# Optimization experiments

Hardware: AMD Instinct MI355X
Metric: run time of the kernel (lower is better)

## Reference

```python
import jax, jax.numpy as jnp
import numpy as np

N = 100000      # num nodes
E = 1600000     # num edges (no self-loops; forward appends N self-loops)
DIN = 256       # in_channels
H = 1           # heads
C = 64          # out_channels per head
NEG = 0.2       # leaky_relu negative slope
NID = N // 10   # number of ID nodes


def setup_inputs() -> dict:
    key = jax.random.key(0)
    ks = jax.random.split(key, 7)
    x = jax.random.normal(ks[0], (N, DIN), jnp.float32)
    src = jax.random.randint(ks[1], (E,), 0, N, dtype=jnp.int32)
    off = jax.random.randint(ks[2], (E,), 1, N, dtype=jnp.int32)
    dst = ((src.astype(jnp.int64) + off.astype(jnp.int64)) % N).astype(jnp.int32)  # guarantees no self-loops
    edge_index = jnp.stack([src, dst])  # [2, E], row0 = source j, row1 = target i
    node_id = jax.random.randint(ks[3], (NID,), 0, N, dtype=jnp.int32)
    g = float(1.0 / np.sqrt(DIN))  # glorot-ish scale
    W = jax.random.uniform(ks[4], (DIN, H * C), jnp.float32, -g, g)
    W_id = jax.random.uniform(ks[5], (DIN, H * C), jnp.float32, -g, g)
    att = jax.random.uniform(ks[6], (1, H, 2 * C), jnp.float32, -g, g)
    return dict(x=x, edge_index=edge_index, node_id=node_id, W=W, W_id=W_id, att=att)


def _gat_id_forward(x, W, W_id, att, edge_index, node_id):
    # ID-aware transform: x @ W, plus extra W_id contribution added at id nodes
    x_id = x[node_id] @ W_id                      # [NID, H*C]
    h = x @ W                                     # [N, H*C]
    h = h.at[node_id].add(x_id)
    # add self-loops (inputs contain none)
    loops = jnp.arange(N, dtype=edge_index.dtype)
    src = jnp.concatenate([edge_index[0], loops])  # source j
    dst = jnp.concatenate([edge_index[1], loops])  # target i
    hr = h.reshape(N, H, C)
    xi = hr[dst]                                   # [Et, H, C]
    xj = hr[src]                                   # [Et, H, C]
    # alpha = (cat(x_i, x_j) * att).sum(-1)
    alpha = (xi * att[:, :, :C]).sum(-1) + (xj * att[:, :, C:]).sum(-1)  # [Et, H]
    alpha = jax.nn.leaky_relu(alpha, NEG)
    # segment softmax over target node (every node has a self-loop -> no empty segments)
    m = jax.ops.segment_max(alpha, dst, num_segments=N)
    alpha = jnp.exp(alpha - m[dst])
    s = jax.ops.segment_sum(alpha, dst, num_segments=N)
    alpha = alpha / (s[dst] + 1e-16)
    # dropout p=0 / eval mode -> no-op
    out = jax.ops.segment_sum(xj * alpha[:, :, None], dst, num_segments=N)  # [N, H, C]
    return out.reshape(N, H * C)  # concat=True, bias=False


def reference(x, edge_index, node_id, W, W_id, att):
    return _gat_id_forward(x, W, W_id, att, edge_index, node_id)
```

## Files before the change

### kernel.cpp

```cpp
#include <hip/hip_runtime.h>
#include <hip/hip_bf16.h>

#define N_NODES 100000
#define E_EDGES 1600000
#define DIN 256
#define C_OUT 64
#define NID_CNT 10000
#define NEG 0.2f
#define NBUCK 391
#define CAP 4608
#define GEMM_BLOCKS 782
#define BIN_BLOCKS 242
#define BIN_EPB 6612
#define ID_BLOCKS 79

typedef short bf16x8 __attribute__((ext_vector_type(8)));
typedef float f32x4  __attribute__((ext_vector_type(4)));

__device__ __forceinline__ float lrelu(float x) { return x > 0.f ? x : NEG * x; }
__device__ __forceinline__ unsigned short f2bs(float f) {
    __hip_bfloat16 b = __float2bfloat16(f);
    return *reinterpret_cast<unsigned short*>(&b);
}
__device__ __forceinline__ bf16x8 pack8(float4 a, float4 b) {
    bf16x8 r;
    r[0] = (short)f2bs(a.x); r[1] = (short)f2bs(a.y);
    r[2] = (short)f2bs(a.z); r[3] = (short)f2bs(a.w);
    r[4] = (short)f2bs(b.x); r[5] = (short)f2bs(b.y);
    r[6] = (short)f2bs(b.z); r[7] = (short)f2bs(b.w);
    return r;
}
__device__ __forceinline__ float2 unpk2(unsigned u) {
    return make_float2(__uint_as_float(u << 16), __uint_as_float(u & 0xffff0000u));
}

__global__ __launch_bounds__(256) void k_zero(float* __restrict__ cnt,
                                              int* __restrict__ bkcur) {
    const int t = blockIdx.x * 256 + threadIdx.x;
    if (t < N_NODES) cnt[t] = 0.f;
    if (t < NBUCK) bkcur[t] = t * CAP;
}

__global__ __launch_bounds__(256) void k_prep(const float* __restrict__ W,
                                              const float* __restrict__ Wid,
                                              unsigned short* __restrict__ WtG,
                                              unsigned short* __restrict__ WidtG,
                                              const int* __restrict__ nid,
                                              float* __restrict__ cnt) {
    const int b = blockIdx.x;
    const int tid = threadIdx.x;
    if (b < 128) {
        const int t = b * 256 + tid;
        const int mat = t >> 14;
        const int r = t & 16383;
        const int k = r >> 6, c = r & 63;
        if (mat == 0) WtG[c * DIN + k] = f2bs(W[(long)k * C_OUT + c]);
        else          WidtG[c * DIN + k] = f2bs(Wid[(long)k * C_OUT + c]);
    } else {
        const int t = (b - 128) * 256 + tid;
        if (t < NID_CNT) atomicAdd(&cnt[nid[t]], 1.0f);
    }
}

__global__ __launch_bounds__(512, 8) void k_mega(const float* __restrict__ x,
                                                 const unsigned short* __restrict__ WtG,
                                                 const float* __restrict__ att,
                                                 __hip_bfloat16* __restrict__ hb,
                                                 float* __restrict__ ad,
                                                 float* __restrict__ as,
                                                 const int* __restrict__ ei,
                                                 int* __restrict__ bkcur,
                                                 int2* __restrict__ binned) {
    __shared__ __align__(16) char smem[32768];
    const int blk = blockIdx.x;
    const int tid = threadIdx.x;

    if (blk < GEMM_BLOCKS) {
        char* wlds = smem;
        const int w = tid >> 6, l = tid & 63;
        const int g = l >> 4, cl = l & 15;
        const int r0 = blk * 128;

        #pragma unroll
        for (int i = 0; i < 4; ++i) {
            int f = tid + i * 512;
            int c = f >> 5, s = f & 31;
            int byte = c * 512 + ((s ^ (c & 7)) << 4);
            *(bf16x8*)(wlds + byte) = *(const bf16x8*)(WtG + (long)c * DIN + s * 8);
        }
        __syncthreads();

        f32x4 acc[4] = {};
        const int row0 = r0 + w * 16 + cl;
        const float* xp0 = x + (long)min(row0, N_NODES - 1) * DIN + g * 8;

        float4 xb[2][2];
        xb[0][0] = *(const float4*)(xp0);
        xb[0][1] = *(const float4*)(xp0 + 4);
        #pragma unroll
        for (int kt = 0; kt < 8; ++kt) {
            if (kt < 7) {
                const int nb = (kt + 1) & 1;
                xb[nb][0] = *(const float4*)(xp0 + (kt + 1) * 32);
                xb[nb][1] = *(const float4*)(xp0 + (kt + 1) * 32 + 4);
            }
            const int cb = kt & 1;
            bf16x8 a0 = pack8(xb[cb][0], xb[cb][1]);
            #pragma unroll
            for (int ct = 0; ct < 4; ++ct) {
                int c = ct * 16 + cl;
                int byte = c * 512 + (((kt * 4 + g) ^ (c & 7)) << 4);
                bf16x8 bw = *(const bf16x8*)(wlds + byte);
                acc[ct] = __builtin_amdgcn_mfma_f32_16x16x32_bf16(a0, bw, acc[ct], 0, 0, 0);
            }
        }
        __syncthreads();

        float attv1[4], attv2[4];
        #pragma unroll
        for (int ct = 0; ct < 4; ++ct) {
            attv1[ct] = att[ct * 16 + cl];
            attv2[ct] = att[C_OUT + ct * 16 + cl];
        }
        unsigned short* hbt = (unsigned short*)smem;
        #pragma unroll
        for (int reg = 0; reg < 4; ++reg) {
            const int rbl = w * 16 + g * 4 + reg;
            float pd = 0.f, ps = 0.f;
            #pragma unroll
            for (int ct = 0; ct < 4; ++ct) {
                float hv = acc[ct][reg];
                pd += hv * attv1[ct];
                ps += hv * attv2[ct];
                hbt[rbl * 72 + ct * 16 + cl] = f2bs(hv);
            }
            #pragma unroll
            for (int o = 1; o < 16; o <<= 1) {
                pd += __shfl_xor(pd, o, 64);
                ps += __shfl_xor(ps, o, 64);
            }
            if (cl == 0) {
                int grow = r0 + rbl;
                if (grow < N_NODES) { ad[grow] = pd; as[grow] = ps; }
            }
        }
        __syncthreads();
        #pragma unroll
        for (int i = 0; i < 2; ++i) {
            int f = tid + i * 512;
            int row = f >> 3, s = f & 7;
            int grow = r0 + row;
            if (grow < N_NODES) {
                bf16x8 v = *(const bf16x8*)(smem + row * 144 + s * 16);
                *(bf16x8*)((unsigned short*)hb + (long)grow * C_OUT + s * 8) = v;
            }
        }
    } else {
        int* cnt_s = (int*)smem;
        int* base  = cnt_s + NBUCK;
        int* lcur  = base + NBUCK;
        const int b2 = blk - GEMM_BLOCKS;
        const int e0 = b2 * BIN_EPB;
        const int e1 = min(e0 + BIN_EPB, E_EDGES);
        for (int i = tid; i < NBUCK; i += 512) cnt_s[i] = 0;
        __syncthreads();
        for (int e = e0 + tid; e < e1; e += 512)
            atomicAdd(&cnt_s[ei[E_EDGES + e] >> 8], 1);
        __syncthreads();
        for (int i = tid; i < NBUCK; i += 512) {
            base[i] = cnt_s[i] ? atomicAdd(&bkcur[i], cnt_s[i]) : 0;
            lcur[i] = 0;
        }
        __syncthreads();
        for (int e = e0 + tid; e < e1; e += 512) {
            int s = ei[e];
            int d = ei[E_EDGES + e];
            int bb = d >> 8;
            int r = atomicAdd(&lcur[bb], 1);
            binned[base[bb] + r] = make_int2(s, d);
        }
    }
}

__global__ __launch_bounds__(256) void k_gemm_id(const float* __restrict__ x,
                                                 const unsigned short* __restrict__ WtG,
                                                 const unsigned short* __restrict__ WidtG,
                                                 const float* __restrict__ cnt,
                                                 const int* __restrict__ nid,
                                                 const float* __restrict__ att,
                                                 __hip_bfloat16* __restrict__ hb,
                                                 float* __restrict__ ad,
                                                 float* __restrict__ as) {
    __shared__ __align__(16) char wlds[65536];
    __shared__ int nodes[128];
    __shared__ float cvs[128];
    const int tid = threadIdx.x;
    const int w = tid >> 6, l = tid & 63;
    const int g = l >> 4, cl = l & 15;
    const int r0 = blockIdx.x * 128;
    if (tid < 128) {
        int idx = r0 + tid;
        int nd = (idx < NID_CNT) ? nid[idx] : -1;
        nodes[tid] = nd;
        cvs[tid] = (nd >= 0) ? cnt[nd] : 0.f;
    }
    #pragma unroll
    for (int i = 0; i < 16; ++i) {
        int f = tid + i * 256;
        int half = f >> 11;
        int ff = f & 2047;
        int c = ff >> 5, s = ff & 31;
        int byte = half * 32768 + c * 512 + ((s ^ (c & 7)) << 4);
        const unsigned short* src = half ? WidtG : WtG;
        *(bf16x8*)(wlds + byte) = *(const bf16x8*)(src + (long)c * DIN + s * 8);
    }
    __syncthreads();

    const int n0 = nodes[w * 32 + cl];
    const int n1 = nodes[w * 32 + 16 + cl];
    const float* xp0 = x + (long)max(n0, 0) * DIN + g * 8;
    const float* xp1 = x + (long)max(n1, 0) * DIN + g * 8;

    f32x4 acc1[2][4] = {};
    f32x4 acc2[2][4] = {};
    #pragma unroll
    for (int kt = 0; kt < 8; ++kt) {
        float4 u0 = *(const float4*)(xp0 + kt * 32);
        float4 u1 = *(const float4*)(xp0 + kt * 32 + 4);
        float4 v0 = *(const float4*)(xp1 + kt * 32);
        float4 v1 = *(const float4*)(xp1 + kt * 32 + 4);
        bf16x8 a0 = pack8(u0, u1);
        bf16x8 a1 = pack8(v0, v1);
        #pragma unroll
        for (int ct = 0; ct < 4; ++ct) {
            int c = ct * 16 + cl;
            int byte = c * 512 + (((kt * 4 + g) ^ (c & 7)) << 4);
            bf16x8 bw = *(const bf16x8*)(wlds + byte);
            bf16x8 bi = *(const bf16x8*)(wlds + 32768 + byte);
            acc1[0][ct] = __builtin_amdgcn_mfma_f32_16x16x32_bf16(a0, bw, acc1[0][ct], 0, 0, 0);
            acc1[1][ct] = __builtin_amdgcn_mfma_f32_16x16x32_bf16(a1, bw, acc1[1][ct], 0, 0, 0);
            acc2[0][ct] = __builtin_amdgcn_mfma_f32_16x16x32_bf16(a0, bi, acc2[0][ct], 0, 0, 0);
            acc2[1][ct] = __builtin_amdgcn_mfma_f32_16x16x32_bf16(a1, bi, acc2[1][ct], 0, 0, 0);
        }
    }
    __syncthreads();

    float attv1[4], attv2[4];
    #pragma unroll
    for (int ct = 0; ct < 4; ++ct) {
        attv1[ct] = att[ct * 16 + cl];
        attv2[ct] = att[C_OUT + ct * 16 + cl];
    }
    unsigned short* hbt = (unsigned short*)wlds;
    #pragma unroll
    for (int rt = 0; rt < 2; ++rt) {
        #pragma unroll
        for (int reg = 0; reg < 4; ++reg) {
            const int rbl = w * 32 + rt * 16 + g * 4 + reg;
            const float cv = cvs[rbl];
            float pd = 0.f, ps = 0.f;
            #pragma unroll
            for (int ct = 0; ct < 4; ++ct) {
                float hv = acc1[rt][ct][reg] + cv * acc2[rt][ct][reg];
                pd += hv * attv1[ct];
                ps += hv * attv2[ct];
                hbt[rbl * 72 + ct * 16 + cl] = f2bs(hv);
            }
            #pragma unroll
            for (int o = 1; o < 16; o <<= 1) {
                pd += __shfl_xor(pd, o, 64);
                ps += __shfl_xor(ps, o, 64);
            }
            if (cl == 0) {
                int nd = nodes[rbl];
                if (nd >= 0) { ad[nd] = pd; as[nd] = ps; }
            }
        }
    }
    __syncthreads();
    #pragma unroll
    for (int i = 0; i < 4; ++i) {
        int f = tid + i * 256;
        int row = f >> 3, s = f & 7;
        int nd = nodes[row];
        if (nd >= 0) {
            bf16x8 v = *(const bf16x8*)(wlds + row * 144 + s * 16);
            *(bf16x8*)((unsigned short*)hb + (long)nd * C_OUT + s * 8) = v;
        }
    }
}

__global__ __launch_bounds__(256) void k_place(const int2* __restrict__ binned,
                                               const int* __restrict__ bkcur,
                                               int* __restrict__ csr,
                                               int* __restrict__ cur) {
    __shared__ int ncnt[256];
    __shared__ int tmp[256];
    __shared__ int ncur[256];
    const int tid = threadIdx.x;
    const int b = blockIdx.x;
    const int lo = b * CAP;
    const int n = bkcur[b] - lo;
    const int node0 = b << 8;
    ncnt[tid] = 0;
    __syncthreads();
    for (int e = tid; e < n; e += 256)
        atomicAdd(&ncnt[binned[lo + e].y - node0], 1);
    __syncthreads();
    const int v = ncnt[tid];
    tmp[tid] = v;
    __syncthreads();
    for (int o = 1; o < 256; o <<= 1) {
        int t = (tid >= o) ? tmp[tid - o] : 0;
        __syncthreads();
        tmp[tid] += t;
        __syncthreads();
    }
    const int incl = tmp[tid];
    if (node0 + tid < N_NODES) cur[node0 + tid] = lo + incl;
    ncur[tid] = incl - v;
    __syncthreads();
    for (int e = tid; e < n; e += 256) {
        int2 p = binned[lo + e];
        int r = atomicAdd(&ncur[p.y - node0], 1);
        csr[lo + r] = p.x;
    }
}

__global__ __launch_bounds__(256) void k_gather(const int* __restrict__ cur,
                                                const int* __restrict__ csr,
                                                const unsigned* __restrict__ hb2,
                                                const float* __restrict__ ad,
                                                const float* __restrict__ as,
                                                float* __restrict__ out) {
    const int lane = threadIdx.x & 63;
    const int lg = lane & 31;
    const int gb = lane & 32;
    const int i = blockIdx.x * 8 + ((threadIdx.x >> 6) << 1) + (lane >> 5);
    if (i >= N_NODES) return;
    const int end   = cur[i];
    const int start = (i & 255) ? cur[i - 1] : (i >> 8) * CAP;
    const int deg   = end - start;
    const float adi = ad[i];
    const float asi = as[i];
    float2 acc;
    float den;
    if (deg <= 32) {
        int s = 0; float a = -1e30f;
        if (lg < deg) { s = csr[start + lg]; a = as[s]; }
        float mx = fmaxf(a, asi);
        #pragma unroll
        for (int o = 16; o > 0; o >>= 1) mx = fmaxf(mx, __shfl_xor(mx, o, 64));
        const float m = lrelu(adi + mx);
        float w = (lg < deg) ? __expf(lrelu(adi + a) - m) : 0.f;
        const float wself = __expf(lrelu(adi + asi) - m);
        float wsum = w;
        #pragma unroll
        for (int o = 16; o > 0; o >>= 1) wsum += __shfl_xor(wsum, o, 64);
        den = wself + wsum;
        float2 hv = unpk2(hb2[(long)i * 32 + lg]);
        acc = make_float2(wself * hv.x, wself * hv.y);
        int j = 0;
        for (; j + 4 <= deg; j += 4) {
            int   s0 = __shfl(s, gb + j, 64),     s1 = __shfl(s, gb + j + 1, 64),
                  s2 = __shfl(s, gb + j + 2, 64), s3 = __shfl(s, gb + j + 3, 64);
            float w0 = __shfl(w, gb + j, 64),     w1 = __shfl(w, gb + j + 1, 64),
                  w2 = __shfl(w, gb + j + 2, 64), w3 = __shfl(w, gb + j + 3, 64);
            float2 h0 = unpk2(hb2[(long)s0 * 32 + lg]);
            float2 h1 = unpk2(hb2[(long)s1 * 32 + lg]);
            float2 h2 = unpk2(hb2[(long)s2 * 32 + lg]);
            float2 h3 = unpk2(hb2[(long)s3 * 32 + lg]);
            acc.x += w0 * h0.x; acc.y += w0 * h0.y;
            acc.x += w1 * h1.x; acc.y += w1 * h1.y;
            acc.x += w2 * h2.x; acc.y += w2 * h2.y;
            acc.x += w3 * h3.x; acc.y += w3 * h3.y;
        }
        for (; j < deg; ++j) {
            int   sj = __shfl(s, gb + j, 64);
            float wj = __shfl(w, gb + j, 64);
            float2 hj = unpk2(hb2[(long)sj * 32 + lg]);
            acc.x += wj * hj.x; acc.y += wj * hj.y;
        }
    } else {
        float mx = asi;
        for (int b = 0; b < deg; b += 32) {
            int idx = b + lg;
            if (idx < deg) mx = fmaxf(mx, as[csr[start + idx]]);
        }
        #pragma unroll
        for (int o = 16; o > 0; o >>= 1) mx = fmaxf(mx, __shfl_xor(mx, o, 64));
        const float m = lrelu(adi + mx);
        const float wself = __expf(lrelu(adi + asi) - m);
        float2 hv = unpk2(hb2[(long)i * 32 + lg]);
        acc = make_float2(wself * hv.x, wself * hv.y);
        den = wself;
        for (int b = 0; b < deg; b += 32) {
            int idx = b + lg;
            int s = 0; float w = 0.f;
            if (idx < deg) {
                s = csr[start + idx];
                w = __expf(lrelu(adi + as[s]) - m);
            }
            const int cnt2 = min(32, deg - b);
            for (int j = 0; j < cnt2; ++j) {
                int   sj = __shfl(s, gb + j, 64);
                float wj = __shfl(w, gb + j, 64);
                float2 hj = unpk2(hb2[(long)sj * 32 + lg]);
                acc.x += wj * hj.x; acc.y += wj * hj.y;
            }
            float wsum = w;
            #pragma unroll
            for (int o = 16; o > 0; o >>= 1) wsum += __shfl_xor(wsum, o, 64);
            den += wsum;
        }
    }
    const float r = 1.f / (den + 1e-16f);
    *(float2*)(out + (long)i * C_OUT + lg * 2) = make_float2(acc.x * r, acc.y * r);
}

extern "C" void kernel_launch(void* const* d_in, const int* in_sizes, int n_in,
                              void* d_out, int out_size, void* d_ws, size_t ws_size,
                              hipStream_t stream) {
    const float* x   = (const float*)d_in[0];
    const int*   ei  = (const int*)d_in[1];
    const int*   nid = (const int*)d_in[2];
    const float* W   = (const float*)d_in[3];
    const float* Wid = (const float*)d_in[4];
    const float* att = (const float*)d_in[5];
    float* out = (float*)d_out;

    char* ws = (char*)d_ws;
    __hip_bfloat16* hb = (__hip_bfloat16*)(ws);
    float* ad    = (float*)(ws + 12800000);
    float* as    = (float*)(ws + 13200000);
    float* cnt   = (float*)(ws + 13600000);
    int*   cur   = (int*)  (ws + 14000000);
    int2*  binned = (int2*)(ws + 14400000);
    int*   csr   = (int*)  (ws + 28900000);
    unsigned short* WtG  = (unsigned short*)(ws + 36200000);
    unsigned short* WidG = (unsigned short*)(ws + 36232768);
    int*   bkcur = (int*)  (ws + 36265536);

    k_zero<<<393, 256, 0, stream>>>(cnt, bkcur);
    k_prep<<<168, 256, 0, stream>>>(W, Wid, WtG, WidG, nid, cnt);
    k_mega<<<GEMM_BLOCKS + BIN_BLOCKS, 512, 0, stream>>>(x, WtG, att, hb, ad, as,
                                                         ei, bkcur, binned);
    k_gemm_id<<<ID_BLOCKS, 256, 0, stream>>>(x, WtG, WidG, cnt, nid, att, hb, ad, as);
    k_place<<<NBUCK, 256, 0, stream>>>(binned, bkcur, csr, cur);
    k_gather<<<12500, 256, 0, stream>>>(cur, csr, (const unsigned*)hb, ad, as, out);
}
```

Measured before the change: 119.0 us.

## Stage x tiles through LDS with double buffering and compact binned edges

```diff
diff --git a/kernel.cpp b/kernel.cpp
--- a/kernel.cpp
+++ b/kernel.cpp
@@ -10,8 +10,9 @@
 #define NBUCK 391
 #define CAP 4608
 #define GEMM_BLOCKS 782
-#define BIN_BLOCKS 242
-#define BIN_EPB 6612
+#define BIN_BLOCKS 121
+#define BIN_EPB 13224
+#define BIN_ITERS 26
 #define ID_BLOCKS 79
 
 typedef short bf16x8 __attribute__((ext_vector_type(8)));
@@ -21,6 +22,12 @@
 __device__ __forceinline__ unsigned short f2bs(float f) {
     __hip_bfloat16 b = __float2bfloat16(f);
     return *reinterpret_cast<unsigned short*>(&b);
+}
+__device__ __forceinline__ uint2 pack4(float4 v) {
+    uint2 r;
+    r.x = ((unsigned)f2bs(v.y) << 16) | f2bs(v.x);
+    r.y = ((unsigned)f2bs(v.w) << 16) | f2bs(v.z);
+    return r;
 }
 __device__ __forceinline__ bf16x8 pack8(float4 a, float4 b) {
     bf16x8 r;
@@ -62,7 +69,7 @@
     }
 }
 
-__global__ __launch_bounds__(512, 8) void k_mega(const float* __restrict__ x,
+__global__ __launch_bounds__(512, 4) void k_mega(const float* __restrict__ x,
                                                  const unsigned short* __restrict__ WtG,
                                                  const float* __restrict__ att,
                                                  __hip_bfloat16* __restrict__ hb,
@@ -70,17 +77,55 @@
                                                  float* __restrict__ as,
                                                  const int* __restrict__ ei,
                                                  int* __restrict__ bkcur,
-                                                 int2* __restrict__ binned) {
-    __shared__ __align__(16) char smem[32768];
+                                                 unsigned* __restrict__ binned) {
+    __shared__ __align__(16) char smem[65536];
     const int blk = blockIdx.x;
     const int tid = threadIdx.x;
 
     if (blk < GEMM_BLOCKS) {
         char* wlds = smem;
+        char* xt   = smem + 32768;
         const int w = tid >> 6, l = tid & 63;
         const int g = l >> 4, cl = l & 15;
+        const int sr  = tid >> 4;
+        const int seg = tid & 15;
         const int r0 = blk * 128;
 
+        #define XLOAD(v0, v1, v2, v3, kc)                                              \
+            v0 = *(const float4*)(x + (long)min(r0 + sr,      N_NODES - 1) * DIN + (kc) * 64 + seg * 4); \
+            v1 = *(const float4*)(x + (long)min(r0 + sr + 32, N_NODES - 1) * DIN + (kc) * 64 + seg * 4); \
+            v2 = *(const float4*)(x + (long)min(r0 + sr + 64, N_NODES - 1) * DIN + (kc) * 64 + seg * 4); \
+            v3 = *(const float4*)(x + (long)min(r0 + sr + 96, N_NODES - 1) * DIN + (kc) * 64 + seg * 4)
+
+        #define XWRITE(v0, v1, v2, v3, buf)                                            \
+            {                                                                          \
+                char* bp = xt + (buf) * 16384;                                         \
+                *(uint2*)(bp + (sr)      * 128 + (((seg >> 1) ^ (sr & 7)) << 4)        + (seg & 1) * 8) = pack4(v0); \
+                *(uint2*)(bp + (sr + 32) * 128 + (((seg >> 1) ^ ((sr + 32) & 7)) << 4) + (seg & 1) * 8) = pack4(v1); \
+                *(uint2*)(bp + (sr + 64) * 128 + (((seg >> 1) ^ ((sr + 64) & 7)) << 4) + (seg & 1) * 8) = pack4(v2); \
+                *(uint2*)(bp + (sr + 96) * 128 + (((seg >> 1) ^ ((sr + 96) & 7)) << 4) + (seg & 1) * 8) = pack4(v3); \
+            }
+
+        const int arow = w * 16 + cl;
+        const int ax = arow & 7;
+        f32x4 acc[4] = {};
+
+        #define XCOMPUTE(buf, kc)                                                      \
+            _Pragma("unroll")                                                          \
+            for (int kt = 0; kt < 2; ++kt) {                                           \
+                bf16x8 a0 = *(const bf16x8*)(xt + (buf) * 16384 + arow * 128 +         \
+                                             (((kt * 4 + g) ^ ax) << 4));              \
+                _Pragma("unroll")                                                      \
+                for (int ct = 0; ct < 4; ++ct) {                                       \
+                    int c = ct * 16 + cl;                                              \
+                    int slot = (kc) * 8 + kt * 4 + g;                                  \
+                    bf16x8 bw = *(const bf16x8*)(wlds + c * 512 + ((slot ^ (c & 7)) << 4)); \
+                    acc[ct] = __builtin_amdgcn_mfma_f32_16x16x32_bf16(a0, bw, acc[ct], 0, 0, 0); \
+                }                                                                      \
+            }
+
+        float4 a0v, a1v, a2v, a3v, b0v, b1v, b2v, b3v;
+        XLOAD(a0v, a1v, a2v, a3v, 0);
         #pragma unroll
         for (int i = 0; i < 4; ++i) {
             int f = tid + i * 512;
@@ -88,32 +133,21 @@
             int byte = c * 512 + ((s ^ (c & 7)) << 4);
             *(bf16x8*)(wlds + byte) = *(const bf16x8*)(WtG + (long)c * DIN + s * 8);
         }
-        __syncthreads();
-
-        f32x4 acc[4] = {};
-        const int row0 = r0 + w * 16 + cl;
-        const float* xp0 = x + (long)min(row0, N_NODES - 1) * DIN + g * 8;
-
-        float4 xb[2][2];
-        xb[0][0] = *(const float4*)(xp0);
-        xb[0][1] = *(const float4*)(xp0 + 4);
-        #pragma unroll
-        for (int kt = 0; kt < 8; ++kt) {
-            if (kt < 7) {
-                const int nb = (kt + 1) & 1;
-                xb[nb][0] = *(const float4*)(xp0 + (kt + 1) * 32);
-                xb[nb][1] = *(const float4*)(xp0 + (kt + 1) * 32 + 4);
-            }
-            const int cb = kt & 1;
-            bf16x8 a0 = pack8(xb[cb][0], xb[cb][1]);
-            #pragma unroll
-            for (int ct = 0; ct < 4; ++ct) {
-                int c = ct * 16 + cl;
-                int byte = c * 512 + (((kt * 4 + g) ^ (c & 7)) << 4);
-                bf16x8 bw = *(const bf16x8*)(wlds + byte);
-                acc[ct] = __builtin_amdgcn_mfma_f32_16x16x32_bf16(a0, bw, acc[ct], 0, 0, 0);
-            }
-        }
+        XWRITE(a0v, a1v, a2v, a3v, 0);
+        XLOAD(b0v, b1v, b2v, b3v, 1);
+        __syncthreads();
+        XCOMPUTE(0, 0);
+        XWRITE(b0v, b1v, b2v, b3v, 1);
+        XLOAD(a0v, a1v, a2v, a3v, 2);
+        __syncthreads();
+        XCOMPUTE(1, 1);
+        XWRITE(a0v, a1v, a2v, a3v, 0);
+        XLOAD(b0v, b1v, b2v, b3v, 3);
+        __syncthreads();
+        XCOMPUTE(0, 2);
+        XWRITE(b0v, b1v, b2v, b3v, 1);
+        __syncthreads();
+        XCOMPUTE(1, 3);
         __syncthreads();
 
         float attv1[4], attv2[4];
@@ -122,7 +156,7 @@
             attv1[ct] = att[ct * 16 + cl];
             attv2[ct] = att[C_OUT + ct * 16 + cl];
         }
-        unsigned short* hbt = (unsigned short*)smem;
+        unsigned short* hbt = (unsigned short*)wlds;
         #pragma unroll
         for (int reg = 0; reg < 4; ++reg) {
             const int rbl = w * 16 + g * 4 + reg;
@@ -151,10 +185,13 @@
             int row = f >> 3, s = f & 7;
             int grow = r0 + row;
             if (grow < N_NODES) {
-                bf16x8 v = *(const bf16x8*)(smem + row * 144 + s * 16);
+                bf16x8 v = *(const bf16x8*)(wlds + row * 144 + s * 16);
                 *(bf16x8*)((unsigned short*)hb + (long)grow * C_OUT + s * 8) = v;
             }
         }
+        #undef XLOAD
+        #undef XWRITE
+        #undef XCOMPUTE
     } else {
         int* cnt_s = (int*)smem;
         int* base  = cnt_s + NBUCK;
@@ -164,20 +201,29 @@
         const int e1 = min(e0 + BIN_EPB, E_EDGES);
         for (int i = tid; i < NBUCK; i += 512) cnt_s[i] = 0;
         __syncthreads();
-        for (int e = e0 + tid; e < e1; e += 512)
-            atomicAdd(&cnt_s[ei[E_EDGES + e] >> 8], 1);
+        int se[BIN_ITERS], de[BIN_ITERS];
+        #pragma unroll
+        for (int j = 0; j < BIN_ITERS; ++j) {
+            int e = e0 + j * 512 + tid;
+            if (e < e1) {
+                se[j] = ei[e];
+                de[j] = ei[E_EDGES + e];
+                atomicAdd(&cnt_s[de[j] >> 8], 1);
+            } else de[j] = -1;
+        }
         __syncthreads();
         for (int i = tid; i < NBUCK; i += 512) {
             base[i] = cnt_s[i] ? atomicAdd(&bkcur[i], cnt_s[i]) : 0;
             lcur[i] = 0;
         }
         __syncthreads();
-        for (int e = e0 + tid; e < e1; e += 512) {
-            int s = ei[e];
-            int d = ei[E_EDGES + e];
-            int bb = d >> 8;
-            int r = atomicAdd(&lcur[bb], 1);
-            binned[base[bb] + r] = make_int2(s, d);
+        #pragma unroll
+        for (int j = 0; j < BIN_ITERS; ++j) {
+            if (de[j] >= 0) {
+                int bb = de[j] >> 8;
+                int r = atomicAdd(&lcur[bb], 1);
+                binned[base[bb] + r] = ((unsigned)se[j] << 8) | (unsigned)(de[j] & 255);
+            }
         }
     }
 }
@@ -290,7 +336,7 @@
     }
 }
 
-__global__ __launch_bounds__(256) void k_place(const int2* __restrict__ binned,
+__global__ __launch_bounds__(256) void k_place(const unsigned* __restrict__ binned,
                                                const int* __restrict__ bkcur,
                                                int* __restrict__ csr,
                                                int* __restrict__ cur) {
@@ -305,7 +351,7 @@
     ncnt[tid] = 0;
     __syncthreads();
     for (int e = tid; e < n; e += 256)
-        atomicAdd(&ncnt[binned[lo + e].y - node0], 1);
+        atomicAdd(&ncnt[binned[lo + e] & 255u], 1);
     __syncthreads();
     const int v = ncnt[tid];
     tmp[tid] = v;
@@ -321,9 +367,9 @@
     ncur[tid] = incl - v;
     __syncthreads();
     for (int e = tid; e < n; e += 256) {
-        int2 p = binned[lo + e];
-        int r = atomicAdd(&ncur[p.y - node0], 1);
-        csr[lo + r] = p.x;
+        unsigned p = binned[lo + e];
+        int r = atomicAdd(&ncur[p & 255u], 1);
+        csr[lo + r] = (int)(p >> 8);
     }
 }
 
@@ -435,11 +481,11 @@
     float* as    = (float*)(ws + 13200000);
     float* cnt   = (float*)(ws + 13600000);
     int*   cur   = (int*)  (ws + 14000000);
-    int2*  binned = (int2*)(ws + 14400000);
-    int*   csr   = (int*)  (ws + 28900000);
-    unsigned short* WtG  = (unsigned short*)(ws + 36200000);
-    unsigned short* WidG = (unsigned short*)(ws + 36232768);
-    int*   bkcur = (int*)  (ws + 36265536);
+    unsigned* binned = (unsigned*)(ws + 14400000);
+    int*   csr   = (int*)  (ws + 21700000);
+    unsigned short* WtG  = (unsigned short*)(ws + 29000000);
+    unsigned short* WidG = (unsigned short*)(ws + 29032768);
+    int*   bkcur = (int*)  (ws + 29065536);
 
     k_zero<<<393, 256, 0, stream>>>(cnt, bkcur);
     k_prep<<<168, 256, 0, stream>>>(W, Wid, WtG, WidG, nid, cnt);
```

New measurement: 123.1 us. +3.5%, slower.
